# Kernel tuning notes

Measured on AMD Instinct MI355X. Metric: run time of the kernel, lower is better.

The kernel has to match this reference:

```python
import jax, jax.numpy as jnp
import numpy as np

B, Cin, C, H, W = 2, 64, 128, 64, 64
D_INNER, N_STATE, DT_RANK, K = 256, 16, 8, 4


def _silu(x):
    return x * jax.nn.sigmoid(x)


def _layernorm(x, g, b, eps=1e-5):
    mu = x.mean(-1, keepdims=True)
    var = ((x - mu) ** 2).mean(-1, keepdims=True)
    return (x - mu) * jax.lax.rsqrt(var + eps) * g + b


def setup_inputs():
    key = jax.random.key(0)
    ks = jax.random.split(key, 16)
    f32 = jnp.float32
    inp = {}
    inp["x"] = jax.random.normal(ks[0], (B, Cin, H, W), f32)
    inp["convin_w"] = jax.random.normal(ks[1], (C, Cin), f32) * 0.05
    inp["convin_b"] = jnp.zeros((C,), f32)
    inp["ln_g"] = jnp.ones((C,), f32)
    inp["ln_b"] = jnp.zeros((C,), f32)
    inp["in_proj_w"] = jax.random.normal(ks[2], (2 * D_INNER, C), f32) * 0.05
    inp["conv_w"] = jax.random.normal(ks[3], (D_INNER, 1, 3, 3), f32) * 0.1
    inp["conv_b"] = jnp.zeros((D_INNER,), f32)
    inp["x_proj_w"] = jax.random.normal(ks[4], (K, DT_RANK + 2 * N_STATE, D_INNER), f32) * 0.05
    inp["dt_w"] = jax.random.normal(ks[5], (K, D_INNER, DT_RANK), f32) * 0.1
    inp["dt_b"] = jax.random.uniform(ks[6], (K, D_INNER), f32, -4.0, -1.0)
    inp["A_logs"] = jnp.log(jnp.tile(jnp.arange(1, N_STATE + 1, dtype=f32), (K, D_INNER, 1)))
    inp["Ds"] = jnp.ones((K, D_INNER), f32)
    inp["outnorm_g"] = jnp.ones((D_INNER,), f32)
    inp["outnorm_b"] = jnp.zeros((D_INNER,), f32)
    inp["out_proj_w"] = jax.random.normal(ks[7], (C, D_INNER), f32) * 0.05
    inp["ca_fc1_w"] = jax.random.normal(ks[8], (C // 16, C), f32) * 0.1
    inp["ca_fc2_w"] = jax.random.normal(ks[9], (C, C // 16), f32) * 0.1
    inp["gn_g"] = jnp.ones((C,), f32)
    inp["gn_b"] = jnp.zeros((C,), f32)
    return inp


def _selective_scan(u, delta, A, Bm, Cm, Ds):
    # u, delta: (B,K,d,L); A: (K,d,N); Bm, Cm: (B,K,N,L); Ds: (K,d)
    def step(h, inp):
        u_t, dt, B_t, C_t = inp
        dA = jnp.exp(dt[..., None] * A)                      # (B,K,d,N)
        h = h * dA + dt[..., None] * B_t[:, :, None, :] * u_t[..., None]
        y = jnp.einsum('bkdn,bkn->bkd', h, C_t)
        return h, y
    step = jax.checkpoint(step)
    seq = (jnp.moveaxis(u, -1, 0), jnp.moveaxis(delta, -1, 0),
           jnp.moveaxis(Bm, -1, 0), jnp.moveaxis(Cm, -1, 0))
    h0 = jnp.zeros(u.shape[:3] + (A.shape[-1],), u.dtype)
    _, ys = jax.lax.scan(step, h0, seq)                      # (L,B,K,d)
    y = jnp.moveaxis(ys, 0, -1)                              # (B,K,d,L)
    return y + u * Ds[None, :, :, None]


def reference(x, convin_w, convin_b, ln_g, ln_b, in_proj_w, conv_w, conv_b,
              x_proj_w, dt_w, dt_b, A_logs, Ds, outnorm_g, outnorm_b,
              out_proj_w, ca_fc1_w, ca_fc2_w, gn_g, gn_b):
    L = H * W
    # 1x1 conv in
    x1 = jnp.einsum('bchw,oc->bohw', x, convin_w) + convin_b[None, :, None, None]
    m = x1.transpose(0, 2, 3, 1)                             # (B,H,W,C)
    # VSSBlock: LN -> SS2D -> residual
    m_ln = _layernorm(m, ln_g, ln_b)
    xz = m_ln @ in_proj_w.T                                  # (B,H,W,2*d_inner)
    xm, z = jnp.split(xz, 2, axis=-1)
    xm = xm.transpose(0, 3, 1, 2)                            # (B,d,H,W)
    xm = jax.lax.conv_general_dilated(xm, conv_w, (1, 1), [(1, 1), (1, 1)],
                                      feature_group_count=D_INNER)
    xm = _silu(xm + conv_b[None, :, None, None])
    x_flat = xm.reshape(B, D_INNER, L)
    x_tr = xm.transpose(0, 1, 3, 2).reshape(B, D_INNER, L)
    xs = jnp.stack([x_flat, x_tr, jnp.flip(x_flat, -1), jnp.flip(x_tr, -1)], axis=1)
    x_dbl = jnp.einsum('bkdl,kcd->bkcl', xs, x_proj_w)
    dts, Bs, Cs = jnp.split(x_dbl, [DT_RANK, DT_RANK + N_STATE], axis=2)
    delta = jax.nn.softplus(jnp.einsum('bkrl,kdr->bkdl', dts, dt_w) + dt_b[None, :, :, None])
    A = -jnp.exp(A_logs)                                     # (K,d,N)
    out_y = _selective_scan(xs, delta, A, Bs, Cs, Ds)        # (B,4,d,L)
    y0 = out_y[:, 0]
    y1 = out_y[:, 1].reshape(B, D_INNER, W, H).transpose(0, 1, 3, 2).reshape(B, D_INNER, L)
    y2 = jnp.flip(out_y[:, 2], -1)
    y3 = jnp.flip(out_y[:, 3], -1).reshape(B, D_INNER, W, H).transpose(0, 1, 3, 2).reshape(B, D_INNER, L)
    y = (y0 + y1 + y2 + y3).transpose(0, 2, 1).reshape(B, H, W, D_INNER)
    y = _layernorm(y, outnorm_g, outnorm_b)
    y = y * _silu(z)
    m_out = m + y @ out_proj_w.T                             # (B,H,W,C)
    mamba = m_out.transpose(0, 3, 1, 2)                      # (B,C,H,W)
    # CBAM-style channel attention
    def mlp(v):
        return jax.nn.relu(v @ ca_fc1_w.T) @ ca_fc2_w.T
    avg = mamba.mean((2, 3))
    mx = mamba.max((2, 3))
    att = jax.nn.sigmoid(mlp(avg) + mlp(mx))[:, :, None, None]
    ca = mamba * att
    # GroupNorm(2 groups) + SiLU + residual
    g = ca.reshape(B, 2, -1)
    mu = g.mean(-1, keepdims=True)
    var = ((g - mu) ** 2).mean(-1, keepdims=True)
    g = ((g - mu) * jax.lax.rsqrt(var + 1e-5)).reshape(B, C, H, W)
    g = g * gn_g[None, :, None, None] + gn_b[None, :, None, None]
    return _silu(g) + x1
```

## Files before the change

kernel.cpp:

```cpp
#include <hip/hip_runtime.h>
#include <math.h>


#define DEV __device__ __forceinline__

typedef __attribute__((ext_vector_type(8))) short bf16x8;
typedef __attribute__((ext_vector_type(4))) float f32x4;

DEV float sigm_(float x){ return 1.f/(1.f+__expf(-x)); }
DEV float silu_(float x){ return x*sigm_(x); }
DEV float sp_(float x){ return (x>15.f)? x : __logf(1.f+__expf(x)); }

DEV unsigned short f2bf(float f){
  union{float f; unsigned u;} v; v.f=f;
  unsigned r=v.u + 0x7FFFu + ((v.u>>16)&1u);
  return (unsigned short)(r>>16);
}
DEV float bf2f(unsigned short h){ union{unsigned u; float f;} v; v.u=((unsigned)h)<<16; return v.f; }

DEV int pos_dir(int k, int l){
  switch(k&3){
    case 0: return l;
    case 1: return ((l&63)<<6)|(l>>6);
    case 2: return 4095-l;
    default:{ int m=4095-l; return ((m&63)<<6)|(m>>6); }
  }
}

DEV bf16x8 cvt_frag(const float* p){
  float4 q0=*(const float4*)p, q1=*(const float4*)(p+4);
  bf16x8 t;
  t[0]=(short)f2bf(q0.x); t[1]=(short)f2bf(q0.y); t[2]=(short)f2bf(q0.z); t[3]=(short)f2bf(q0.w);
  t[4]=(short)f2bf(q1.x); t[5]=(short)f2bf(q1.y); t[6]=(short)f2bf(q1.z); t[7]=(short)f2bf(q1.w);
  return t;
}

__global__ __launch_bounds__(256) void k_x1ln(const float* __restrict__ x,
    const float* __restrict__ W, const float* __restrict__ bias,
    const float* __restrict__ g, const float* __restrict__ be,
    float* __restrict__ x1, unsigned short* __restrict__ mlnb){
  const int b=blockIdx.y, p0=blockIdx.x*64;
  __shared__ float sw[64*132];
  __shared__ float sx[64*68];
  __shared__ float red[2][16][68];
  __shared__ float smu[64], srs[64];
  const int tid=threadIdx.x, tx=tid&15, ty=tid>>4;
  for (int i=tid;i<8192;i+=256){ int c=i&63,o=i>>6; sw[c*132+o]=W[o*64+c]; }
  for (int i=tid;i<4096;i+=256){ int c=i>>6,p=i&63; sx[c*68+p]=x[((size_t)(b*64+c))*4096+p0+p]; }
  __syncthreads();
  float acc[8][4]={};
  for (int c=0;c<64;++c){
    float4 a0=*(const float4*)&sw[c*132+ty*8];
    float4 a1=*(const float4*)&sw[c*132+ty*8+4];
    float4 bv=*(const float4*)&sx[c*68+tx*4];
    acc[0][0]=fmaf(a0.x,bv.x,acc[0][0]); acc[0][1]=fmaf(a0.x,bv.y,acc[0][1]); acc[0][2]=fmaf(a0.x,bv.z,acc[0][2]); acc[0][3]=fmaf(a0.x,bv.w,acc[0][3]);
    acc[1][0]=fmaf(a0.y,bv.x,acc[1][0]); acc[1][1]=fmaf(a0.y,bv.y,acc[1][1]); acc[1][2]=fmaf(a0.y,bv.z,acc[1][2]); acc[1][3]=fmaf(a0.y,bv.w,acc[1][3]);
    acc[2][0]=fmaf(a0.z,bv.x,acc[2][0]); acc[2][1]=fmaf(a0.z,bv.y,acc[2][1]); acc[2][2]=fmaf(a0.z,bv.z,acc[2][2]); acc[2][3]=fmaf(a0.z,bv.w,acc[2][3]);
    acc[3][0]=fmaf(a0.w,bv.x,acc[3][0]); acc[3][1]=fmaf(a0.w,bv.y,acc[3][1]); acc[3][2]=fmaf(a0.w,bv.z,acc[3][2]); acc[3][3]=fmaf(a0.w,bv.w,acc[3][3]);
    acc[4][0]=fmaf(a1.x,bv.x,acc[4][0]); acc[4][1]=fmaf(a1.x,bv.y,acc[4][1]); acc[4][2]=fmaf(a1.x,bv.z,acc[4][2]); acc[4][3]=fmaf(a1.x,bv.w,acc[4][3]);
    acc[5][0]=fmaf(a1.y,bv.x,acc[5][0]); acc[5][1]=fmaf(a1.y,bv.y,acc[5][1]); acc[5][2]=fmaf(a1.y,bv.z,acc[5][2]); acc[5][3]=fmaf(a1.y,bv.w,acc[5][3]);
    acc[6][0]=fmaf(a1.z,bv.x,acc[6][0]); acc[6][1]=fmaf(a1.z,bv.y,acc[6][1]); acc[6][2]=fmaf(a1.z,bv.z,acc[6][2]); acc[6][3]=fmaf(a1.z,bv.w,acc[6][3]);
    acc[7][0]=fmaf(a1.w,bv.x,acc[7][0]); acc[7][1]=fmaf(a1.w,bv.y,acc[7][1]); acc[7][2]=fmaf(a1.w,bv.z,acc[7][2]); acc[7][3]=fmaf(a1.w,bv.w,acc[7][3]);
  }
  float xr[8][4];
  #pragma unroll
  for (int i=0;i<8;++i){
    float bs=bias[ty*8+i];
    #pragma unroll
    for (int j=0;j<4;++j) xr[i][j]=acc[i][j]+bs;
  }
  {
    float s[4]={},s2[4]={};
    #pragma unroll
    for (int i=0;i<8;++i)
      #pragma unroll
      for (int j=0;j<4;++j){ s[j]+=xr[i][j]; s2[j]=fmaf(xr[i][j],xr[i][j],s2[j]); }
    #pragma unroll
    for (int j=0;j<4;++j){ red[0][ty][tx*4+j]=s[j]; red[1][ty][tx*4+j]=s2[j]; }
  }
  __syncthreads();
  if (tid<64){
    float S=0.f,S2=0.f;
    #pragma unroll
    for (int t=0;t<16;++t){ S+=red[0][t][tid]; S2+=red[1][t][tid]; }
    float mu=S*(1.f/128.f), var=S2*(1.f/128.f)-mu*mu;
    smu[tid]=mu; srs[tid]=rsqrtf(var+1e-5f);
  }
  __syncthreads();
  float* lnt=sw;
  #pragma unroll
  for (int i=0;i<8;++i){
    int o=ty*8+i;
    float gv=g[o], bev=be[o];
    #pragma unroll
    for (int j=0;j<4;++j){
      int p=tx*4+j;
      lnt[o*66+p]=(xr[i][j]-smu[p])*srs[p]*gv+bev;
    }
    *(float4*)&x1[((size_t)(b*128+o))*4096+p0+tx*4]=make_float4(xr[i][0],xr[i][1],xr[i][2],xr[i][3]);
  }
  __syncthreads();
  for (int i=tid;i<8192;i+=256){ int p=i>>7,o=i&127; mlnb[((size_t)(b*4096+p0+p))*128+o]=f2bf(lnt[o*66+p]); }
}

__global__ __launch_bounds__(256) void k_inproj(const unsigned short* __restrict__ mlnb,
    const float* __restrict__ W, unsigned short* __restrict__ xmpreb, float* __restrict__ z){
  const int wave=threadIdx.x>>6, lane=threadIdx.x&63;
  const int quad=lane>>4, l16=lane&15;
  const int m0=blockIdx.y*128+(wave>>1)*64;
  const int n0=blockIdx.x*64+(wave&1)*32;
  f32x4 acc[4][2];
  #pragma unroll
  for (int i=0;i<4;++i)
    #pragma unroll
    for (int j=0;j<2;++j) acc[i][j]=(f32x4){0.f,0.f,0.f,0.f};
  for (int k0=0;k0<128;k0+=32){
    bf16x8 a[4], b[2];
    #pragma unroll
    for (int mi=0;mi<4;++mi)
      a[mi]=*(const bf16x8*)&mlnb[(size_t)(m0+mi*16+l16)*128 + k0 + quad*8];
    #pragma unroll
    for (int ni=0;ni<2;++ni)
      b[ni]=cvt_frag(&W[(size_t)(n0+ni*16+l16)*128 + k0 + quad*8]);
    #pragma unroll
    for (int mi=0;mi<4;++mi)
      #pragma unroll
      for (int ni=0;ni<2;++ni)
        acc[mi][ni]=__builtin_amdgcn_mfma_f32_16x16x32_bf16(a[mi],b[ni],acc[mi][ni],0,0,0);
  }
  #pragma unroll
  for (int mi=0;mi<4;++mi)
    #pragma unroll
    for (int ni=0;ni<2;++ni)
      #pragma unroll
      for (int r=0;r<4;++r){
        const int row=m0+mi*16+quad*4+r;
        const int col=n0+ni*16+l16;
        float v=acc[mi][ni][r];
        if (col<256) xmpreb[(size_t)row*256+col]=f2bf(v);
        else         z[(size_t)row*256+(col-256)]=v;
      }
}

__global__ __launch_bounds__(256) void k_dwconv(const unsigned short* __restrict__ xmpreb,
    const float* __restrict__ cw, const float* __restrict__ cb, unsigned short* __restrict__ xflatb){
  __shared__ float sw[2304];
  __shared__ float sb[256];
  const int tid=threadIdx.x;
  for (int i=tid;i<2304;i+=256) sw[i]=cw[i];
  sb[tid]=cb[tid];
  __syncthreads();
  const int bp0=blockIdx.x*16;
  const int b=bp0>>12, p0=bp0&4095;
  const int dq=tid&63, pg=tid>>6;
  const int d0=dq*4;
  float wr[9][4];
  #pragma unroll
  for (int t=0;t<9;++t)
    #pragma unroll
    for (int c=0;c<4;++c) wr[t][c]=sw[(d0+c)*9+t];
  const float4 bias=make_float4(sb[d0],sb[d0+1],sb[d0+2],sb[d0+3]);
  #pragma unroll
  for (int j=0;j<4;++j){
    const int p=p0+pg*4+j;
    const int h=p>>6, w=p&63;
    float4 acc=bias;
    #pragma unroll
    for (int dh=-1;dh<=1;++dh){
      int hh=h+dh; if ((unsigned)hh>=64u) continue;
      #pragma unroll
      for (int dw=-1;dw<=1;++dw){
        int ww=w+dw; if ((unsigned)ww>=64u) continue;
        const int t=(dh+1)*3+(dw+1);
        ushort4 u4=*(const ushort4*)&xmpreb[((size_t)((b<<12)+hh*64+ww))*256+d0];
        acc.x=fmaf(bf2f(u4.x),wr[t][0],acc.x); acc.y=fmaf(bf2f(u4.y),wr[t][1],acc.y);
        acc.z=fmaf(bf2f(u4.z),wr[t][2],acc.z); acc.w=fmaf(bf2f(u4.w),wr[t][3],acc.w);
      }
    }
    ushort4 o;
    o.x=f2bf(silu_(acc.x)); o.y=f2bf(silu_(acc.y)); o.z=f2bf(silu_(acc.z)); o.w=f2bf(silu_(acc.w));
    *(ushort4*)&xflatb[((size_t)((b<<12)+p))*256+d0]=o;
  }
}

__global__ __launch_bounds__(256) void k_proj(const unsigned short* __restrict__ xflatb,
    const float* __restrict__ xpw, float* __restrict__ pdt, float* __restrict__ pbc){
  const int wave=threadIdx.x>>6, lane=threadIdx.x&63;
  const int quad=lane>>4, l16=lane&15;
  const int m0=(wave&1)*80;
  const int n0=blockIdx.x*32+(wave>>1)*16;
  f32x4 acc[5];
  #pragma unroll
  for (int i=0;i<5;++i) acc[i]=(f32x4){0.f,0.f,0.f,0.f};
  for (int k0=0;k0<256;k0+=32){
    bf16x8 a[5], b;
    #pragma unroll
    for (int mi=0;mi<5;++mi)
      a[mi]=cvt_frag(&xpw[(size_t)(m0+mi*16+l16)*256 + k0 + quad*8]);
    b=*(const bf16x8*)&xflatb[(size_t)(n0+l16)*256 + k0 + quad*8];
    #pragma unroll
    for (int mi=0;mi<5;++mi)
      acc[mi]=__builtin_amdgcn_mfma_f32_16x16x32_bf16(a[mi],b,acc[mi],0,0,0);
  }
  #pragma unroll
  for (int mi=0;mi<5;++mi)
    #pragma unroll
    for (int r=0;r<4;++r){
      const int rr=m0+mi*16+quad*4+r;
      const int col=n0+l16;
      const int b_=col>>12, pos=col&4095;
      const int kd=rr/40, c=rr%40, bk=b_*4+kd;
      float v=acc[mi][r];
      if (c<8) pdt[((size_t)bk*4096+pos)*8+c]=v;
      else     pbc[((size_t)bk*4096+pos)*32+(c-8)]=v;
    }
}

__global__ __launch_bounds__(256) void k_scanA(const float* __restrict__ pdt,
    const float* __restrict__ pbc, const unsigned short* __restrict__ xflatb,
    const float* __restrict__ dtw, const float* __restrict__ dtb,
    const float* __restrict__ A_logs, const float* __restrict__ Ds,
    unsigned short* __restrict__ Pcb, unsigned short* __restrict__ Heb,
    float* __restrict__ ysum){
  const int bx=blockIdx.x;
  const int ch=bx&127, k=(bx>>7)&3, b=bx>>9, bk=b*4+k;
  const int d=threadIdx.x;
  __shared__ float sbc[1024];
  __shared__ float sdt[256];
  for (int i=d;i<1024;i+=256) sbc[i]=pbc[((size_t)bk*4096+(ch<<5))*32+i];
  sdt[d]=pdt[((size_t)bk*4096+(ch<<5))*8+d];
  const float* ap=&A_logs[((k<<8)+d)<<4];
  const float ac0=-__expf(ap[0]);
  bool pw=true;
  #pragma unroll
  for (int n=1;n<16;++n){ float an_=-__expf(ap[n]); pw=pw&&(fabsf(an_-(float)(n+1)*ac0)<=1e-4f*fabsf(an_)); }
  float w8[8];
  {
    float4 w0=*(const float4*)&dtw[(size_t)k*2048+d*8];
    float4 w1=*(const float4*)&dtw[(size_t)k*2048+d*8+4];
    w8[0]=w0.x;w8[1]=w0.y;w8[2]=w0.z;w8[3]=w0.w;w8[4]=w1.x;w8[5]=w1.y;w8[6]=w1.z;w8[7]=w1.w;
  }
  const float dtbd=dtb[(k<<8)+d];
  const float dsv=Ds[(k<<8)+d];
  __syncthreads();
  float h[16]; float sdv=0.f;
  #pragma unroll
  for (int n=0;n<16;++n) h[n]=0.f;
  const unsigned short* up=xflatb+((size_t)b<<12)*256+d;
  if (pw){
    for (int s=0;s<32;++s){
      const int l=(ch<<5)+s;
      float t=dtbd;
      #pragma unroll
      for (int r=0;r<8;++r) t=fmaf(sdt[s*8+r],w8[r],t);
      const float dv=sp_(t);
      const int pos=pos_dir(k,l);
      const float u=bf2f(up[(size_t)pos*256]);
      const float dvu=dv*u;
      sdv+=dv;
      const float q=__expf(dv*ac0);
      float an=q, yl=0.f;
      #pragma unroll
      for (int n4=0;n4<4;++n4){
        float4 bb=*(const float4*)&sbc[s*32+n4*4];
        float4 cc=*(const float4*)&sbc[s*32+16+n4*4];
        h[n4*4+0]=fmaf(h[n4*4+0],an,dvu*bb.x); yl=fmaf(h[n4*4+0],cc.x,yl); an*=q;
        h[n4*4+1]=fmaf(h[n4*4+1],an,dvu*bb.y); yl=fmaf(h[n4*4+1],cc.y,yl); an*=q;
        h[n4*4+2]=fmaf(h[n4*4+2],an,dvu*bb.z); yl=fmaf(h[n4*4+2],cc.z,yl); an*=q;
        h[n4*4+3]=fmaf(h[n4*4+3],an,dvu*bb.w); yl=fmaf(h[n4*4+3],cc.w,yl); an*=q;
      }
      atomicAdd(&ysum[((size_t)((b<<12)+pos))*256+d], yl+u*dsv);
    }
  } else {
    float acoef[16];
    #pragma unroll
    for (int n=0;n<16;++n) acoef[n]=-__expf(ap[n]);
    for (int s=0;s<32;++s){
      const int l=(ch<<5)+s;
      float t=dtbd;
      #pragma unroll
      for (int r=0;r<8;++r) t=fmaf(sdt[s*8+r],w8[r],t);
      const float dv=sp_(t);
      const int pos=pos_dir(k,l);
      const float u=bf2f(up[(size_t)pos*256]);
      const float dvu=dv*u;
      sdv+=dv;
      float yl=0.f;
      #pragma unroll
      for (int n=0;n<16;++n){
        float a=__expf(dv*acoef[n]);
        h[n]=fmaf(h[n],a,dvu*sbc[s*32+n]);
        yl=fmaf(h[n],sbc[s*32+16+n],yl);
      }
      atomicAdd(&ysum[((size_t)((b<<12)+pos))*256+d], yl+u*dsv);
    }
  }
  const size_t obase=(size_t)ch*32768 + ((size_t)bk*256+d)*16;
  if (pw){
    const float qe=__expf(ac0*sdv);
    float an=qe;
    #pragma unroll
    for (int n4=0;n4<4;++n4){
      ushort4 o;
      o.x=f2bf(an); an*=qe; o.y=f2bf(an); an*=qe;
      o.z=f2bf(an); an*=qe; o.w=f2bf(an); an*=qe;
      *(ushort4*)&Pcb[obase+n4*4]=o;
    }
  } else {
    #pragma unroll
    for (int n=0;n<16;++n) Pcb[obase+n]=f2bf(__expf(-__expf(ap[n])*sdv));
  }
  #pragma unroll
  for (int n4=0;n4<4;++n4){
    ushort4 o;
    o.x=f2bf(h[n4*4]); o.y=f2bf(h[n4*4+1]); o.z=f2bf(h[n4*4+2]); o.w=f2bf(h[n4*4+3]);
    *(ushort4*)&Heb[obase+n4*4]=o;
  }
}

__global__ __launch_bounds__(256) void k_scanB(const unsigned short* Pcb,
    const unsigned short* Heb, unsigned short* Hinb){
  const int g2=threadIdx.x&63, tc=threadIdx.x>>6;
  const int gid=blockIdx.x*64+g2;
  float p[32], e[32];
  #pragma unroll
  for (int i=0;i<32;++i){
    size_t idx=(size_t)(tc*32+i)*32768+gid;
    p[i]=bf2f(Pcb[idx]); e[i]=bf2f(Heb[idx]);
  }
  float P=1.f, E=0.f;
  #pragma unroll
  for (int i=0;i<32;++i){ E=fmaf(E,p[i],e[i]); P*=p[i]; }
  __shared__ float sP[4][64], sE[4][64];
  sP[tc][g2]=P; sE[tc][g2]=E;
  __syncthreads();
  float Hp=0.f;
  for (int t=0;t<tc;++t) Hp=fmaf(Hp,sP[t][g2],sE[t][g2]);
  #pragma unroll
  for (int i=0;i<32;++i){
    Hinb[(size_t)(tc*32+i)*32768+gid]=f2bf(Hp);
    Hp=fmaf(Hp,p[i],e[i]);
  }
}

__global__ __launch_bounds__(256) void k_scanC2(const float* __restrict__ pdt,
    const float* __restrict__ pbc, const float* __restrict__ dtw,
    const float* __restrict__ dtb, const float* __restrict__ A_logs,
    const unsigned short* __restrict__ Hinb, float* __restrict__ ysum){
  const int bx=blockIdx.x;
  const int ch=bx&127, k=(bx>>7)&3, b=bx>>9, bk=b*4+k;
  if (ch==0) return;
  const int d=threadIdx.x;
  __shared__ float sC[512];
  __shared__ float sdt[256];
  for (int i=d;i<512;i+=256){ int s=i>>4,n=i&15; sC[i]=pbc[((size_t)bk*4096+(ch<<5)+s)*32+16+n]; }
  sdt[d]=pdt[((size_t)bk*4096+(ch<<5))*8+d];
  const float* ap=&A_logs[((k<<8)+d)<<4];
  const float ac0=-__expf(ap[0]);
  bool pw=true;
  #pragma unroll
  for (int n=1;n<16;++n){ float an_=-__expf(ap[n]); pw=pw&&(fabsf(an_-(float)(n+1)*ac0)<=1e-4f*fabsf(an_)); }
  float w8[8];
  {
    float4 w0=*(const float4*)&dtw[(size_t)k*2048+d*8];
    float4 w1=*(const float4*)&dtw[(size_t)k*2048+d*8+4];
    w8[0]=w0.x;w8[1]=w0.y;w8[2]=w0.z;w8[3]=w0.w;w8[4]=w1.x;w8[5]=w1.y;w8[6]=w1.z;w8[7]=w1.w;
  }
  const float dtbd=dtb[(k<<8)+d];
  __syncthreads();
  const size_t ibase=(size_t)ch*32768 + ((size_t)bk*256+d)*16;
  float h[16];
  #pragma unroll
  for (int n=0;n<16;++n) h[n]=bf2f(Hinb[ibase+n]);
  if (pw){
    float cumd=0.f;
    for (int s=0;s<32;++s){
      float t=dtbd;
      #pragma unroll
      for (int r=0;r<8;++r) t=fmaf(sdt[s*8+r],w8[r],t);
      cumd+=sp_(t);
      const float q=__expf(ac0*cumd);
      float an=q, corr=0.f;
      #pragma unroll
      for (int n4=0;n4<4;++n4){
        float4 cc=*(const float4*)&sC[s*16+n4*4];
        corr=fmaf(h[n4*4+0]*an,cc.x,corr); an*=q;
        corr=fmaf(h[n4*4+1]*an,cc.y,corr); an*=q;
        corr=fmaf(h[n4*4+2]*an,cc.z,corr); an*=q;
        corr=fmaf(h[n4*4+3]*an,cc.w,corr); an*=q;
      }
      const int l=(ch<<5)+s;
      atomicAdd(&ysum[((size_t)((b<<12)+pos_dir(k,l)))*256+d], corr);
    }
  } else {
    float acoef[16];
    #pragma unroll
    for (int n=0;n<16;++n) acoef[n]=-__expf(ap[n]);
    float cumd=0.f;
    for (int s=0;s<32;++s){
      float t=dtbd;
      #pragma unroll
      for (int r=0;r<8;++r) t=fmaf(sdt[s*8+r],w8[r],t);
      cumd+=sp_(t);
      float corr=0.f;
      #pragma unroll
      for (int n=0;n<16;++n) corr=fmaf(h[n]*__expf(acoef[n]*cumd),sC[s*16+n],corr);
      const int l=(ch<<5)+s;
      atomicAdd(&ysum[((size_t)((b<<12)+pos_dir(k,l)))*256+d], corr);
    }
  }
}

__global__ __launch_bounds__(256) void k_outnorm(const float* __restrict__ ysum,
    const float* __restrict__ g, const float* __restrict__ be,
    const float* __restrict__ z, unsigned short* __restrict__ ygb){
  const int bp=blockIdx.x, d=threadIdx.x;
  float v=ysum[(size_t)bp*256+d];
  float s=v, s2=v*v;
  #pragma unroll
  for (int m=1;m<64;m<<=1){ s+=__shfl_xor(s,m); s2+=__shfl_xor(s2,m); }
  __shared__ float rs[4], rs2[4];
  if ((d&63)==0){ rs[d>>6]=s; rs2[d>>6]=s2; }
  __syncthreads();
  float S=rs[0]+rs[1]+rs[2]+rs[3], S2=rs2[0]+rs2[1]+rs2[2]+rs2[3];
  float mu=S*(1.f/256.f), var=S2*(1.f/256.f)-mu*mu, rstd=rsqrtf(var+1e-5f);
  float ln=(v-mu)*rstd*g[d]+be[d];
  float zv=z[(size_t)bp*256+d];
  ygb[(size_t)bp*256+d]=f2bf(ln*silu_(zv));
}

__global__ __launch_bounds__(256) void k_outproj(const unsigned short* __restrict__ ygb,
    const float* __restrict__ W, const float* __restrict__ x1, float* __restrict__ mamba){
  const int wave=threadIdx.x>>6, lane=threadIdx.x&63;
  const int quad=lane>>4, l16=lane&15;
  const int m0=(wave&1)*64;
  const int n0=blockIdx.x*32+(wave>>1)*16;
  f32x4 acc[4];
  #pragma unroll
  for (int i=0;i<4;++i) acc[i]=(f32x4){0.f,0.f,0.f,0.f};
  for (int k0=0;k0<256;k0+=32){
    bf16x8 a[4], b;
    #pragma unroll
    for (int mi=0;mi<4;++mi)
      a[mi]=cvt_frag(&W[(size_t)(m0+mi*16+l16)*256 + k0 + quad*8]);
    b=*(const bf16x8*)&ygb[(size_t)(n0+l16)*256 + k0 + quad*8];
    #pragma unroll
    for (int mi=0;mi<4;++mi)
      acc[mi]=__builtin_amdgcn_mfma_f32_16x16x32_bf16(a[mi],b,acc[mi],0,0,0);
  }
  #pragma unroll
  for (int mi=0;mi<4;++mi)
    #pragma unroll
    for (int r=0;r<4;++r){
      const int c=m0+mi*16+quad*4+r;
      const int col=n0+l16;
      const int b_=col>>12, pos=col&4095;
      const size_t addr=((size_t)((b_<<7)+c))*4096+pos;
      mamba[addr]=acc[mi][r]+x1[addr];
    }
}

__global__ __launch_bounds__(256) void k_stats(const float* __restrict__ mamba, float* __restrict__ stats){
  const int bc=blockIdx.x, tid=threadIdx.x;
  const float* row=mamba+(size_t)bc*4096;
  float s=0.f,s2=0.f,mx=-3.402823466e38f;
  for (int i=tid;i<4096;i+=256){ float v=row[i]; s+=v; s2=fmaf(v,v,s2); mx=fmaxf(mx,v); }
  #pragma unroll
  for (int m=1;m<64;m<<=1){
    s+=__shfl_xor(s,m); s2+=__shfl_xor(s2,m); mx=fmaxf(mx,__shfl_xor(mx,m));
  }
  __shared__ float r0[4],r1[4],r2[4];
  if ((tid&63)==0){ int wv=tid>>6; r0[wv]=s; r1[wv]=s2; r2[wv]=mx; }
  __syncthreads();
  if (tid==0){
    stats[bc*3+0]=r0[0]+r0[1]+r0[2]+r0[3];
    stats[bc*3+1]=r1[0]+r1[1]+r1[2]+r1[3];
    stats[bc*3+2]=fmaxf(fmaxf(r2[0],r2[1]),fmaxf(r2[2],r2[3]));
  }
}

__global__ __launch_bounds__(256) void k_att(const float* __restrict__ stats,
    const float* __restrict__ fc1, const float* __restrict__ fc2,
    float* __restrict__ att, float* __restrict__ gstat){
  __shared__ float avg[2][128], mxs[2][128], S1[2][128], S2[2][128], hsum[2][8], attv[2][128];
  const int tid=threadIdx.x, b=tid>>7, c=tid&127;
  float s1=stats[tid*3], s2=stats[tid*3+1], m=stats[tid*3+2];
  avg[b][c]=s1*(1.f/4096.f); mxs[b][c]=m; S1[b][c]=s1; S2[b][c]=s2;
  __syncthreads();
  if (tid<16){
    int bb=tid>>3, i=tid&7;
    float ha=0.f,hm=0.f;
    for (int cc=0;cc<128;++cc){ float w=fc1[i*128+cc]; ha=fmaf(w,avg[bb][cc],ha); hm=fmaf(w,mxs[bb][cc],hm); }
    hsum[bb][i]=fmaxf(ha,0.f)+fmaxf(hm,0.f);
  }
  __syncthreads();
  float sacc=0.f;
  #pragma unroll
  for (int i=0;i<8;++i) sacc=fmaf(fc2[c*8+i],hsum[b][i],sacc);
  float a=sigm_(sacc);
  attv[b][c]=a; att[tid]=a;
  __syncthreads();
  if (tid<4){
    int bb=tid>>1, gp=tid&1;
    float sum1=0.f,sum2=0.f;
    for (int cc=0;cc<64;++cc){
      int c2=gp*64+cc; float av=attv[bb][c2];
      sum1=fmaf(av,S1[bb][c2],sum1);
      sum2=fmaf(av*av,S2[bb][c2],sum2);
    }
    const float inv=1.f/(64.f*4096.f);
    float mu=sum1*inv, ex2=sum2*inv, var=ex2-mu*mu;
    gstat[tid*2]=mu; gstat[tid*2+1]=rsqrtf(var+1e-5f);
  }
}

__global__ __launch_bounds__(256) void k_final(const float* __restrict__ mamba,
    const float* __restrict__ x1, const float* __restrict__ att,
    const float* __restrict__ gstat, const float* __restrict__ gg,
    const float* __restrict__ gb, float* __restrict__ out){
  const int idx=blockIdx.x*256+threadIdx.x;
  const int c=(idx>>12)&127, b=idx>>19;
  const int grp=(b<<1)+(c>>6);
  float v=mamba[idx]*att[(b<<7)+c];
  float vn=(v-gstat[grp*2])*gstat[grp*2+1]*gg[c]+gb[c];
  out[idx]=silu_(vn)+x1[idx];
}

extern "C" void kernel_launch(void* const* d_in, const int* in_sizes, int n_in,
                              void* d_out, int out_size, void* d_ws, size_t ws_size,
                              hipStream_t stream){
  (void)in_sizes; (void)n_in; (void)out_size; (void)ws_size;
  const float* x        =(const float*)d_in[0];
  const float* convin_w =(const float*)d_in[1];
  const float* convin_b =(const float*)d_in[2];
  const float* ln_g     =(const float*)d_in[3];
  const float* ln_b     =(const float*)d_in[4];
  const float* in_proj_w=(const float*)d_in[5];
  const float* conv_w   =(const float*)d_in[6];
  const float* conv_b   =(const float*)d_in[7];
  const float* x_proj_w =(const float*)d_in[8];
  const float* dt_w     =(const float*)d_in[9];
  const float* dt_b     =(const float*)d_in[10];
  const float* A_logs   =(const float*)d_in[11];
  const float* Ds       =(const float*)d_in[12];
  const float* outnorm_g=(const float*)d_in[13];
  const float* outnorm_b=(const float*)d_in[14];
  const float* out_proj_w=(const float*)d_in[15];
  const float* ca_fc1_w =(const float*)d_in[16];
  const float* ca_fc2_w =(const float*)d_in[17];
  const float* gn_g     =(const float*)d_in[18];
  const float* gn_b     =(const float*)d_in[19];

  float* ws=(float*)d_ws;
  float*          x1     =ws+0;
  float*          z      =ws+1048576;
  unsigned short* xmpreb =(unsigned short*)(ws+3145728);
  unsigned short* mlnb   =(unsigned short*)(ws+5242880);
  unsigned short* xflatb =(unsigned short*)(ws+6291456);
  float*          pdt    =ws+8388608;
  float*          pbc    =ws+8912896;
  unsigned short* Pcb    =(unsigned short*)(ws+10485760);
  unsigned short* Heb    =(unsigned short*)(ws+12582912);
  float*          ysum   =ws+18874368;
  unsigned short* ygb    =(unsigned short*)(ws+3145728);
  float*          mamba  =ws+5242880;
  float*          stats  =ws+27262976;
  float*          att    =stats+768;
  float*          gstat  =att+256;

  const dim3 blk(256);
  hipMemsetAsync(ysum, 0, 2097152*sizeof(float), stream);
  k_x1ln   <<<dim3(64,2),   blk,0,stream>>>(x, convin_w, convin_b, ln_g, ln_b, x1, mlnb);
  k_inproj <<<dim3(8,64),   blk,0,stream>>>(mlnb, in_proj_w, xmpreb, z);
  k_dwconv <<<dim3(512),    blk,0,stream>>>(xmpreb, conv_w, conv_b, xflatb);
  k_proj   <<<dim3(256),    blk,0,stream>>>(xflatb, x_proj_w, pdt, pbc);
  k_scanA  <<<dim3(1024),   blk,0,stream>>>(pdt, pbc, xflatb, dt_w, dt_b, A_logs, Ds, Pcb, Heb, ysum);
  k_scanB  <<<dim3(512),    blk,0,stream>>>(Pcb, Heb, Pcb );
  k_scanC2 <<<dim3(1024),   blk,0,stream>>>(pdt, pbc, dt_w, dt_b, A_logs, Pcb , ysum);
  k_outnorm<<<dim3(8192),   blk,0,stream>>>(ysum, outnorm_g, outnorm_b, z, ygb);
  k_outproj<<<dim3(256),    blk,0,stream>>>(ygb, out_proj_w, x1, mamba);
  k_stats  <<<dim3(256),    blk,0,stream>>>(mamba, stats);
  k_att    <<<dim3(1),      blk,0,stream>>>(stats, ca_fc1_w, ca_fc2_w, att, gstat);
  k_final  <<<dim3(4096),   blk,0,stream>>>(mamba, x1, att, gstat, gn_g, gn_b, (float*)d_out);
}
```

Measured before the change: 253.8 us.

## Fuse output layernorm into out-projection and attention MLP into final kernel

```diff
diff --git a/kernel.cpp b/kernel.cpp
--- a/kernel.cpp
+++ b/kernel.cpp
@@ -411,30 +411,54 @@
   }
 }
 
-__global__ __launch_bounds__(256) void k_outnorm(const float* __restrict__ ysum,
-    const float* __restrict__ g, const float* __restrict__ be,
-    const float* __restrict__ z, unsigned short* __restrict__ ygb){
-  const int bp=blockIdx.x, d=threadIdx.x;
-  float v=ysum[(size_t)bp*256+d];
-  float s=v, s2=v*v;
-  #pragma unroll
-  for (int m=1;m<64;m<<=1){ s+=__shfl_xor(s,m); s2+=__shfl_xor(s2,m); }
-  __shared__ float rs[4], rs2[4];
-  if ((d&63)==0){ rs[d>>6]=s; rs2[d>>6]=s2; }
-  __syncthreads();
-  float S=rs[0]+rs[1]+rs[2]+rs[3], S2=rs2[0]+rs2[1]+rs2[2]+rs2[3];
-  float mu=S*(1.f/256.f), var=S2*(1.f/256.f)-mu*mu, rstd=rsqrtf(var+1e-5f);
-  float ln=(v-mu)*rstd*g[d]+be[d];
-  float zv=z[(size_t)bp*256+d];
-  ygb[(size_t)bp*256+d]=f2bf(ln*silu_(zv));
-}
-
-__global__ __launch_bounds__(256) void k_outproj(const unsigned short* __restrict__ ygb,
-    const float* __restrict__ W, const float* __restrict__ x1, float* __restrict__ mamba){
-  const int wave=threadIdx.x>>6, lane=threadIdx.x&63;
+__global__ __launch_bounds__(256) void k_outproj(const float* __restrict__ ysum,
+    const float* __restrict__ z, const float* __restrict__ ong,
+    const float* __restrict__ onb, const float* __restrict__ W,
+    const float* __restrict__ x1, float* __restrict__ mamba){
+  __shared__ unsigned short ygs[32*264];
+  __shared__ float red[2][32][9];
+  __shared__ float sg[256], sb2[256];
+  const int tid=threadIdx.x;
+  sg[tid]=ong[tid]; sb2[tid]=onb[tid];
+  const int col_l=tid>>3, seg=tid&7;
+  const int col=blockIdx.x*32+col_l;
+  float v[32];
+  {
+    const float* yp=&ysum[(size_t)col*256+seg*32];
+    float s=0.f,s2=0.f;
+    #pragma unroll
+    for (int j=0;j<8;++j){
+      float4 q=*(const float4*)&yp[j*4];
+      v[j*4]=q.x; v[j*4+1]=q.y; v[j*4+2]=q.z; v[j*4+3]=q.w;
+      s+=q.x+q.y+q.z+q.w;
+      s2=fmaf(q.x,q.x,s2); s2=fmaf(q.y,q.y,s2); s2=fmaf(q.z,q.z,s2); s2=fmaf(q.w,q.w,s2);
+    }
+    red[0][col_l][seg]=s; red[1][col_l][seg]=s2;
+  }
+  __syncthreads();
+  float S=0.f,S2=0.f;
+  #pragma unroll
+  for (int t=0;t<8;++t){ S+=red[0][col_l][t]; S2+=red[1][col_l][t]; }
+  const float mu=S*(1.f/256.f), var=S2*(1.f/256.f)-mu*mu, rstd=rsqrtf(var+1e-5f);
+  {
+    const float* zp=&z[(size_t)col*256+seg*32];
+    unsigned short* yo=&ygs[col_l*264+seg*32];
+    #pragma unroll
+    for (int j=0;j<8;++j){
+      float4 zq=*(const float4*)&zp[j*4];
+      ushort4 o;
+      o.x=f2bf(((v[j*4  ]-mu)*rstd*sg[seg*32+j*4  ]+sb2[seg*32+j*4  ])*silu_(zq.x));
+      o.y=f2bf(((v[j*4+1]-mu)*rstd*sg[seg*32+j*4+1]+sb2[seg*32+j*4+1])*silu_(zq.y));
+      o.z=f2bf(((v[j*4+2]-mu)*rstd*sg[seg*32+j*4+2]+sb2[seg*32+j*4+2])*silu_(zq.z));
+      o.w=f2bf(((v[j*4+3]-mu)*rstd*sg[seg*32+j*4+3]+sb2[seg*32+j*4+3])*silu_(zq.w));
+      *(ushort4*)&yo[j*4]=o;
+    }
+  }
+  __syncthreads();
+  const int wave=tid>>6, lane=tid&63;
   const int quad=lane>>4, l16=lane&15;
   const int m0=(wave&1)*64;
-  const int n0=blockIdx.x*32+(wave>>1)*16;
+  const int nl0=(wave>>1)*16;
   f32x4 acc[4];
   #pragma unroll
   for (int i=0;i<4;++i) acc[i]=(f32x4){0.f,0.f,0.f,0.f};
@@ -443,7 +467,7 @@
     #pragma unroll
     for (int mi=0;mi<4;++mi)
       a[mi]=cvt_frag(&W[(size_t)(m0+mi*16+l16)*256 + k0 + quad*8]);
-    b=*(const bf16x8*)&ygb[(size_t)(n0+l16)*256 + k0 + quad*8];
+    b=*(const bf16x8*)&ygs[(nl0+l16)*264 + k0 + quad*8];
     #pragma unroll
     for (int mi=0;mi<4;++mi)
       acc[mi]=__builtin_amdgcn_mfma_f32_16x16x32_bf16(a[mi],b,acc[mi],0,0,0);
@@ -453,8 +477,8 @@
     #pragma unroll
     for (int r=0;r<4;++r){
       const int c=m0+mi*16+quad*4+r;
-      const int col=n0+l16;
-      const int b_=col>>12, pos=col&4095;
+      const int gcol=blockIdx.x*32+nl0+l16;
+      const int b_=gcol>>12, pos=gcol&4095;
       const size_t addr=((size_t)((b_<<7)+c))*4096+pos;
       mamba[addr]=acc[mi][r]+x1[addr];
     }
@@ -479,50 +503,51 @@
   }
 }
 
-__global__ __launch_bounds__(256) void k_att(const float* __restrict__ stats,
+__global__ __launch_bounds__(256) void k_final(const float* __restrict__ mamba,
+    const float* __restrict__ x1, const float* __restrict__ stats,
     const float* __restrict__ fc1, const float* __restrict__ fc2,
-    float* __restrict__ att, float* __restrict__ gstat){
-  __shared__ float avg[2][128], mxs[2][128], S1[2][128], S2[2][128], hsum[2][8], attv[2][128];
-  const int tid=threadIdx.x, b=tid>>7, c=tid&127;
-  float s1=stats[tid*3], s2=stats[tid*3+1], m=stats[tid*3+2];
-  avg[b][c]=s1*(1.f/4096.f); mxs[b][c]=m; S1[b][c]=s1; S2[b][c]=s2;
-  __syncthreads();
-  if (tid<16){
-    int bb=tid>>3, i=tid&7;
+    const float* __restrict__ gg, const float* __restrict__ gb,
+    float* __restrict__ out){
+  const int idx=blockIdx.x*256+threadIdx.x;
+  const int tid=threadIdx.x;
+  const int c=(idx>>12)&127, b=idx>>19;
+  __shared__ float hsum[8];
+  __shared__ float smu, srstd, satt;
+  if (tid<8){
     float ha=0.f,hm=0.f;
-    for (int cc=0;cc<128;++cc){ float w=fc1[i*128+cc]; ha=fmaf(w,avg[bb][cc],ha); hm=fmaf(w,mxs[bb][cc],hm); }
-    hsum[bb][i]=fmaxf(ha,0.f)+fmaxf(hm,0.f);
-  }
-  __syncthreads();
-  float sacc=0.f;
-  #pragma unroll
-  for (int i=0;i<8;++i) sacc=fmaf(fc2[c*8+i],hsum[b][i],sacc);
-  float a=sigm_(sacc);
-  attv[b][c]=a; att[tid]=a;
-  __syncthreads();
-  if (tid<4){
-    int bb=tid>>1, gp=tid&1;
-    float sum1=0.f,sum2=0.f;
-    for (int cc=0;cc<64;++cc){
-      int c2=gp*64+cc; float av=attv[bb][c2];
-      sum1=fmaf(av,S1[bb][c2],sum1);
-      sum2=fmaf(av*av,S2[bb][c2],sum2);
-    }
-    const float inv=1.f/(64.f*4096.f);
-    float mu=sum1*inv, ex2=sum2*inv, var=ex2-mu*mu;
-    gstat[tid*2]=mu; gstat[tid*2+1]=rsqrtf(var+1e-5f);
-  }
-}
-
-__global__ __launch_bounds__(256) void k_final(const float* __restrict__ mamba,
-    const float* __restrict__ x1, const float* __restrict__ att,
-    const float* __restrict__ gstat, const float* __restrict__ gg,
-    const float* __restrict__ gb, float* __restrict__ out){
-  const int idx=blockIdx.x*256+threadIdx.x;
-  const int c=(idx>>12)&127, b=idx>>19;
-  const int grp=(b<<1)+(c>>6);
-  float v=mamba[idx]*att[(b<<7)+c];
-  float vn=(v-gstat[grp*2])*gstat[grp*2+1]*gg[c]+gb[c];
+    for (int cc=0;cc<128;++cc){
+      float w=fc1[tid*128+cc];
+      const float* st=&stats[((b<<7)+cc)*3];
+      ha=fmaf(w,st[0]*(1.f/4096.f),ha);
+      hm=fmaf(w,st[2],hm);
+    }
+    hsum[tid]=fmaxf(ha,0.f)+fmaxf(hm,0.f);
+  }
+  __syncthreads();
+  if (tid<64){
+    const int cg=((c>>6)<<6)+tid;
+    float a=0.f;
+    #pragma unroll
+    for (int i=0;i<8;++i) a=fmaf(fc2[cg*8+i],hsum[i],a);
+    a=sigm_(a);
+    const float* st=&stats[((b<<7)+cg)*3];
+    float sum1=a*st[0];
+    float sum2=a*a*st[1];
+    #pragma unroll
+    for (int m=1;m<64;m<<=1){ sum1+=__shfl_xor(sum1,m); sum2+=__shfl_xor(sum2,m); }
+    if (tid==0){
+      const float inv=1.f/(64.f*4096.f);
+      float mu=sum1*inv, ex2=sum2*inv;
+      smu=mu; srstd=rsqrtf(ex2-mu*mu+1e-5f);
+      float ao=0.f;
+      #pragma unroll
+      for (int i=0;i<8;++i) ao=fmaf(fc2[c*8+i],hsum[i],ao);
+      satt=sigm_(ao);
+    }
+  }
+  __syncthreads();
+  float v=mamba[idx]*satt;
+  float vn=(v-smu)*srstd*gg[c]+gb[c];
   out[idx]=silu_(vn)+x1[idx];
 }
 
@@ -562,11 +587,8 @@
   unsigned short* Pcb    =(unsigned short*)(ws+10485760);
   unsigned short* Heb    =(unsigned short*)(ws+12582912);
   float*          ysum   =ws+18874368;
-  unsigned short* ygb    =(unsigned short*)(ws+3145728);
   float*          mamba  =ws+5242880;
   float*          stats  =ws+27262976;
-  float*          att    =stats+768;
-  float*          gstat  =att+256;
 
   const dim3 blk(256);
   hipMemsetAsync(ysum, 0, 2097152*sizeof(float), stream);
@@ -577,9 +599,7 @@
   k_scanA  <<<dim3(1024),   blk,0,stream>>>(pdt, pbc, xflatb, dt_w, dt_b, A_logs, Ds, Pcb, Heb, ysum);
   k_scanB  <<<dim3(512),    blk,0,stream>>>(Pcb, Heb, Pcb );
   k_scanC2 <<<dim3(1024),   blk,0,stream>>>(pdt, pbc, dt_w, dt_b, A_logs, Pcb , ysum);
-  k_outnorm<<<dim3(8192),   blk,0,stream>>>(ysum, outnorm_g, outnorm_b, z, ygb);
-  k_outproj<<<dim3(256),    blk,0,stream>>>(ygb, out_proj_w, x1, mamba);
+  k_outproj<<<dim3(256),    blk,0,stream>>>(ysum, z, outnorm_g, outnorm_b, out_proj_w, x1, mamba);
   k_stats  <<<dim3(256),    blk,0,stream>>>(mamba, stats);
-  k_att    <<<dim3(1),      blk,0,stream>>>(stats, ca_fc1_w, ca_fc2_w, att, gstat);
-  k_final  <<<dim3(4096),   blk,0,stream>>>(mamba, x1, att, gstat, gn_g, gn_b, (float*)d_out);
-}
+  k_final  <<<dim3(4096),   blk,0,stream>>>(mamba, x1, stats, ca_fc1_w, ca_fc2_w, gn_g, gn_b, (float*)d_out);
+}
```

Measured after the change: 262.8 us. 1.04x slower.
